# Optimization experiments

Hardware: AMD Instinct MI355X
Metric: run time of the kernel (lower is better)

The kernel has to match this reference:

```python
import jax, jax.numpy as jnp
import numpy as np

N, C, H, W = 32, 256, 56, 56
LN_EPS = 1e-5


def make_dct_filters(c, h, w):
    # Multi-spectral DCT pooling filters (FcaNet-style), bnumfre=4 frequency pairs,
    # channels split into 4 equal groups. DctCFea source unavailable; this is the
    # standard implementation pattern for such a module.
    freqs = [(0, 0), (0, 1), (1, 0), (1, 1)]
    cpf = c // len(freqs)
    f = np.zeros((c, h, w), np.float32)
    for i, (u, v) in enumerate(freqs):
        bh = np.cos(np.pi * u * (np.arange(h) + 0.5) / h) / np.sqrt(h)
        if u != 0:
            bh = bh * np.sqrt(2.0)
        bw = np.cos(np.pi * v * (np.arange(w) + 0.5) / w) / np.sqrt(w)
        if v != 0:
            bw = bw * np.sqrt(2.0)
        f[i * cpf:(i + 1) * cpf] = (bh[:, None] * bw[None, :]).astype(np.float32)
    return jnp.asarray(f)


DCT_F = make_dct_filters(C, H, W)  # (C,H,W) constant buffer


def _ln(s, g, b):
    # LayerNorm over the channel dim (normalized_shape [C,1] / [C,1,1] -> stats over C)
    mu = s.mean(axis=1, keepdims=True)
    var = ((s - mu) ** 2).mean(axis=1, keepdims=True)
    return (s - mu) * jax.lax.rsqrt(var + LN_EPS) * g + b


def setup_inputs() -> dict:
    key = jax.random.key(0)
    ks = jax.random.split(key, 8)
    return {
        "x": jax.random.normal(ks[0], (N, C, H, W), dtype=jnp.float32),
        "gc_w": jax.random.normal(ks[1], (C,), dtype=jnp.float32) * 0.02,
        "gc_b": jnp.zeros((), dtype=jnp.float32),
        "lc_w": jax.random.normal(ks[2], (3,), dtype=jnp.float32) * 0.3,
        "lc_b": jnp.zeros((), dtype=jnp.float32),
        "lcln_g": jnp.ones((C,), dtype=jnp.float32),
        "lcln_b": jnp.zeros((C,), dtype=jnp.float32),
        "tw_w": jax.random.normal(ks[3], (C, C), dtype=jnp.float32) * 0.02,
        "tw_b": jnp.zeros((C,), dtype=jnp.float32),
        "twln_g": jnp.ones((C,), dtype=jnp.float32),
        "twln_b": jnp.zeros((C,), dtype=jnp.float32),
        "wdct": jnp.full((C,), 0.5, dtype=jnp.float32),
        "wmax": jnp.full((C,), 0.5, dtype=jnp.float32),
    }


def reference(x, gc_w, gc_b, lc_w, lc_b, lcln_g, lcln_b, tw_w, tw_b, twln_g, twln_b, wdct, wmax):
    n, c, h, w = x.shape
    xf = x.reshape(n, c, h * w)                                   # (N,C,HW)
    # global context: 1x1 conv to 1 channel, softmax over space, weighted spatial sum
    logits = jnp.einsum('ncs,c->ns', xf, gc_w) + gc_b             # (N,HW)
    attn = jax.nn.softmax(logits, axis=-1)
    x_g = jnp.einsum('ncs,ns->nc', xf, attn)                      # (N,C)
    # pooled stats: max pool + DCT multi-spectral pool, learned blend
    x_max = xf.max(axis=-1)                                       # (N,C)
    x_dct = jnp.einsum('nchw,chw->nc', x, DCT_F)                  # (N,C)
    x_s = wmax * x_max + wdct * x_dct                             # (N,C)
    # local conv1d (k=3, pad=1) across the channel axis
    p = jnp.pad(x_s, ((0, 0), (1, 1)))
    x_l = lc_w[0] * p[:, :-2] + lc_w[1] * p[:, 1:-1] + lc_w[2] * p[:, 2:] + lc_b
    # LayerNorm over channels, 1x1 transform, LayerNorm, sigmoid gate
    att = _ln(x_g + x_s + x_l, lcln_g, lcln_b)                    # (N,C)
    att = att @ tw_w.T + tw_b                                     # tw: 1x1 conv C->C
    gate = jax.nn.sigmoid(_ln(att, twln_g, twln_b))               # (N,C)
    return x * gate[:, :, None, None]
```

## Files before the change

### kernel.cpp

```cpp
#include <hip/hip_runtime.h>
#include <math.h>


#define N_ 32
#define C_ 256
#define H_ 56
#define W_ 56
#define S_ 3136
#define Q_ 784
#define LN_EPS 1e-5f

#define NCH 8
#define CPC 32

using f4 = __attribute__((ext_vector_type(4))) float;

__device__ __forceinline__ float wave_sum(float v) {
  #pragma unroll
  for (int o = 32; o > 0; o >>= 1) v += __shfl_xor(v, o);
  return v;
}
__device__ __forceinline__ float wave_max(float v) {
  #pragma unroll
  for (int o = 32; o > 0; o >>= 1) v = fmaxf(v, __shfl_xor(v, o));
  return v;
}
__device__ __forceinline__ float block_sum(float v, float* red) {
  int lane = threadIdx.x & 63, wid = threadIdx.x >> 6;
  float w = wave_sum(v);
  __syncthreads();
  if (lane == 0) red[wid] = w;
  __syncthreads();
  return red[0] + red[1] + red[2] + red[3];
}
__device__ __forceinline__ float dot4(f4 a, f4 b) {
  return a.x * b.x + a.y * b.y + a.z * b.z + a.w * b.w;
}
__device__ __forceinline__ float max4(f4 a) {
  return fmaxf(fmaxf(a.x, a.y), fmaxf(a.z, a.w));
}

__global__ void k_logits(const float* __restrict__ x, const float* __restrict__ gc_w,
                         float* __restrict__ lpart) {
  int ch = blockIdx.x, n = blockIdx.y, tid = threadIdx.x;
  int c0 = ch * CPC;
  __shared__ float gw[CPC];
  if (tid < CPC) gw[tid] = gc_w[c0 + tid];
  __syncthreads();
  const f4* xb = (const f4*)(x + ((size_t)n * C_ + c0) * S_);
  f4 a0 = {0,0,0,0}, a1 = {0,0,0,0}, a2 = {0,0,0,0};
  #pragma unroll 8
  for (int c = 0; c < CPC; ++c) {
    const f4* xp = xb + (size_t)c * Q_;
    float w = gw[c];
    a0 += w * xp[tid];
    a1 += w * xp[tid + 256];
    a2 += w * xp[tid + 512];
  }
  f4* lp = (f4*)lpart + ((size_t)n * NCH + ch) * Q_;
  lp[tid] = a0; lp[tid + 256] = a1; lp[tid + 512] = a2;
  if (tid < 16) {
    f4 a3 = {0,0,0,0};
    #pragma unroll 8
    for (int c = 0; c < CPC; ++c) a3 += gw[c] * xb[(size_t)c * Q_ + 768 + tid];
    lp[768 + tid] = a3;
  }
}

__global__ void k_softmax(const float* __restrict__ lpart, float* __restrict__ attn) {
  int n = blockIdx.x, tid = threadIdx.x;
  __shared__ float red[4];
  const f4* lp = (const f4*)lpart + (size_t)n * NCH * Q_;
  f4 v[4];
  float m = -INFINITY;
  #pragma unroll
  for (int k = 0; k < 3; ++k) {
    int q = tid + k * 256;
    f4 acc = {0,0,0,0};
    #pragma unroll
    for (int ch = 0; ch < NCH; ++ch) acc += lp[(size_t)ch * Q_ + q];
    v[k] = acc;
    m = fmaxf(m, max4(acc));
  }
  if (tid < 16) {
    f4 acc = {0,0,0,0};
    #pragma unroll
    for (int ch = 0; ch < NCH; ++ch) acc += lp[(size_t)ch * Q_ + 768 + tid];
    v[3] = acc;
    m = fmaxf(m, max4(acc));
  } else {
    v[3] = f4{-INFINITY, -INFINITY, -INFINITY, -INFINITY};
  }
  float wm = wave_max(m);
  int lane = tid & 63, wid = tid >> 6;
  if (lane == 0) red[wid] = wm;
  __syncthreads();
  m = fmaxf(fmaxf(red[0], red[1]), fmaxf(red[2], red[3]));
  float z = 0.f;
  #pragma unroll
  for (int k = 0; k < 4; ++k) {
    v[k].x = expf(v[k].x - m); v[k].y = expf(v[k].y - m);
    v[k].z = expf(v[k].z - m); v[k].w = expf(v[k].w - m);
    z += v[k].x + v[k].y + v[k].z + v[k].w;
  }
  z = block_sum(z, red);
  float inv = 1.f / z;
  f4* ap = (f4*)attn + (size_t)n * Q_;
  #pragma unroll
  for (int k = 0; k < 3; ++k) ap[tid + k * 256] = v[k] * inv;
  if (tid < 16) ap[768 + tid] = v[3] * inv;
}

__global__ void k_stats(const float* __restrict__ x, const float* __restrict__ attn,
                        float* __restrict__ xg, float* __restrict__ xmax,
                        float* __restrict__ xdct) {
  int c = blockIdx.x, n = blockIdx.y, tid = threadIdx.x;
  __shared__ float bh[H_];
  __shared__ f4 bw4[14];
  __shared__ float red[3][4];
  int grp = c >> 6;
  int u = grp >> 1, vv = grp & 1;
  const float invs = 0.13363062f;
  const float sq2  = 1.41421356f;
  if (tid < H_) {
    float b = cosf((float)M_PI * u * (tid + 0.5f) / H_) * invs;
    bh[tid] = u ? b * sq2 : b;
  } else if (tid >= 64 && tid < 64 + 14) {
    int j = tid - 64;
    f4 b;
    #pragma unroll
    for (int e = 0; e < 4; ++e) {
      float t = cosf((float)M_PI * vv * (4 * j + e + 0.5f) / W_) * invs;
      ((float*)&b)[e] = vv ? t * sq2 : t;
    }
    bw4[j] = b;
  }
  __syncthreads();
  const f4* xp = (const f4*)(x + ((size_t)n * C_ + c) * S_);
  const f4* ap = (const f4*)(attn + (size_t)n * S_);
  float g = 0.f, d = 0.f, mx = -INFINITY;
  #pragma unroll
  for (int k = 0; k < 3; ++k) {
    int q = tid + k * 256;
    f4 xv = xp[q], av = ap[q];
    g += dot4(xv, av);
    mx = fmaxf(max4(xv), mx);
    int h = q / 14;
    d += bh[h] * dot4(xv, bw4[q - h * 14]);
  }
  if (tid < 16) {
    int q = 768 + tid;
    f4 xv = xp[q], av = ap[q];
    g += dot4(xv, av);
    mx = fmaxf(max4(xv), mx);
    int h = q / 14;
    d += bh[h] * dot4(xv, bw4[q - h * 14]);
  }
  float gs = wave_sum(g), ms = wave_max(mx), ds = wave_sum(d);
  int lane = tid & 63, wid = tid >> 6;
  if (lane == 0) { red[0][wid] = gs; red[1][wid] = ms; red[2][wid] = ds; }
  __syncthreads();
  if (tid == 0) {
    xg[n * C_ + c]   = red[0][0] + red[0][1] + red[0][2] + red[0][3];
    xmax[n * C_ + c] = fmaxf(fmaxf(red[1][0], red[1][1]), fmaxf(red[1][2], red[1][3]));
    xdct[n * C_ + c] = red[2][0] + red[2][1] + red[2][2] + red[2][3];
  }
}

__global__ void k_gate(const float* __restrict__ xg, const float* __restrict__ xmax,
                       const float* __restrict__ xdct,
                       const float* __restrict__ lc_w, const float* __restrict__ lc_b,
                       const float* __restrict__ lcln_g, const float* __restrict__ lcln_b,
                       const float* __restrict__ tw_w, const float* __restrict__ tw_b,
                       const float* __restrict__ twln_g, const float* __restrict__ twln_b,
                       const float* __restrict__ wdct, const float* __restrict__ wmax,
                       float* __restrict__ gate) {
  int n = blockIdx.x, c = threadIdx.x;
  __shared__ float xs[C_ + 2];
  __shared__ float att_s[C_];
  __shared__ float red[4];
  float g  = xg[n * C_ + c];
  float sv = wmax[c] * xmax[n * C_ + c] + wdct[c] * xdct[n * C_ + c];
  xs[c + 1] = sv;
  if (c == 0) { xs[0] = 0.f; xs[C_ + 1] = 0.f; }
  __syncthreads();
  float xl = lc_w[0] * xs[c] + lc_w[1] * xs[c + 1] + lc_w[2] * xs[c + 2] + lc_b[0];
  float t = g + sv + xl;
  float mu  = block_sum(t, red) * (1.f / C_);
  float dv  = t - mu;
  float var = block_sum(dv * dv, red) * (1.f / C_);
  float att = dv * rsqrtf(var + LN_EPS) * lcln_g[c] + lcln_b[c];
  att_s[c] = att;
  __syncthreads();
  float a2 = tw_b[c];
  const f4* wrow = (const f4*)(tw_w + c * C_);
  const f4* arow = (const f4*)att_s;
  #pragma unroll 8
  for (int k = 0; k < C_ / 4; ++k) a2 += dot4(wrow[k], arow[k]);
  float mu2  = block_sum(a2, red) * (1.f / C_);
  float d2   = a2 - mu2;
  float var2 = block_sum(d2 * d2, red) * (1.f / C_);
  float z = d2 * rsqrtf(var2 + LN_EPS) * twln_g[c] + twln_b[c];
  gate[n * C_ + c] = 1.f / (1.f + expf(-z));
}

__global__ void k_scale(const float* __restrict__ x, const float* __restrict__ gate,
                        float* __restrict__ out) {
  const f4* x4 = (const f4*)x;
  f4* o4 = (f4*)out;
  const int total = N_ * C_ * Q_;
  for (int i = blockIdx.x * blockDim.x + threadIdx.x; i < total;
       i += gridDim.x * blockDim.x) {
    int nc = i / Q_;
    float gv = gate[nc];
    f4 v = x4[i];
    v *= gv;
    o4[i] = v;
  }
}

extern "C" void kernel_launch(void* const* d_in, const int* in_sizes, int n_in,
                              void* d_out, int out_size, void* d_ws, size_t ws_size,
                              hipStream_t stream) {
  const float* x      = (const float*)d_in[0];
  const float* gc_w   = (const float*)d_in[1];
  const float* lc_w   = (const float*)d_in[3];
  const float* lc_b   = (const float*)d_in[4];
  const float* lcln_g = (const float*)d_in[5];
  const float* lcln_b = (const float*)d_in[6];
  const float* tw_w   = (const float*)d_in[7];
  const float* tw_b   = (const float*)d_in[8];
  const float* twln_g = (const float*)d_in[9];
  const float* twln_b = (const float*)d_in[10];
  const float* wdct   = (const float*)d_in[11];
  const float* wmax   = (const float*)d_in[12];
  float* out = (float*)d_out;

  float* ws    = (float*)d_ws;
  float* lpart = ws;
  float* attn  = lpart + (size_t)NCH * N_ * S_;
  float* xg    = attn + (size_t)N_ * S_;
  float* xmax_ = xg + N_ * C_;
  float* xdct_ = xmax_ + N_ * C_;
  float* gate  = xdct_ + N_ * C_;

  hipLaunchKernelGGL(k_logits, dim3(NCH, N_), dim3(256), 0, stream, x, gc_w, lpart);
  hipLaunchKernelGGL(k_softmax, dim3(N_), dim3(256), 0, stream, lpart, attn);
  hipLaunchKernelGGL(k_stats, dim3(C_, N_), dim3(256), 0, stream, x, attn, xg, xmax_, xdct_);
  hipLaunchKernelGGL(k_gate, dim3(N_), dim3(256), 0, stream,
                     xg, xmax_, xdct_, lc_w, lc_b, lcln_g, lcln_b,
                     tw_w, tw_b, twln_g, twln_b, wdct, wmax, gate);
  hipLaunchKernelGGL(k_scale, dim3(2048), dim3(256), 0, stream, x, gate, out);
}
```

Measured before the change: 88.90 us.

## Fuse all stages into one persistent kernel with software grid barriers

```diff
diff --git a/kernel.cpp b/kernel.cpp
--- a/kernel.cpp
+++ b/kernel.cpp
@@ -10,8 +10,10 @@
 #define Q_ 784
 #define LN_EPS 1e-5f
 
-#define NCH 8
-#define CPC 32
+#define NCH 16
+#define CPC 16
+#define GRID 512
+#define NTHR 256
 
 using f4 = __attribute__((ext_vector_type(4))) float;
 
@@ -40,182 +42,196 @@
   return fmaxf(fmaxf(a.x, a.y), fmaxf(a.z, a.w));
 }
 
-__global__ void k_logits(const float* __restrict__ x, const float* __restrict__ gc_w,
-                         float* __restrict__ lpart) {
-  int ch = blockIdx.x, n = blockIdx.y, tid = threadIdx.x;
-  int c0 = ch * CPC;
-  __shared__ float gw[CPC];
-  if (tid < CPC) gw[tid] = gc_w[c0 + tid];
-  __syncthreads();
-  const f4* xb = (const f4*)(x + ((size_t)n * C_ + c0) * S_);
-  f4 a0 = {0,0,0,0}, a1 = {0,0,0,0}, a2 = {0,0,0,0};
-  #pragma unroll 8
-  for (int c = 0; c < CPC; ++c) {
-    const f4* xp = xb + (size_t)c * Q_;
-    float w = gw[c];
-    a0 += w * xp[tid];
-    a1 += w * xp[tid + 256];
-    a2 += w * xp[tid + 512];
-  }
-  f4* lp = (f4*)lpart + ((size_t)n * NCH + ch) * Q_;
-  lp[tid] = a0; lp[tid + 256] = a1; lp[tid + 512] = a2;
-  if (tid < 16) {
-    f4 a3 = {0,0,0,0};
+__device__ __forceinline__ void grid_bar(unsigned* bar, unsigned target) {
+  __syncthreads();
+  if (threadIdx.x == 0) {
+    __threadfence();
+    __hip_atomic_fetch_add(bar, 1u, __ATOMIC_RELAXED, __HIP_MEMORY_SCOPE_AGENT);
+    while (__hip_atomic_load(bar, __ATOMIC_RELAXED, __HIP_MEMORY_SCOPE_AGENT) < target)
+      __builtin_amdgcn_s_sleep(2);
+    __threadfence();
+  }
+  __syncthreads();
+}
+
+__global__ __launch_bounds__(NTHR, 2)
+void k_fused(const float* __restrict__ x, const float* __restrict__ gc_w,
+             const float* __restrict__ lc_w, const float* __restrict__ lc_b,
+             const float* __restrict__ lcln_g, const float* __restrict__ lcln_b,
+             const float* __restrict__ tw_w, const float* __restrict__ tw_b,
+             const float* __restrict__ twln_g, const float* __restrict__ twln_b,
+             const float* __restrict__ wdct, const float* __restrict__ wmax,
+             float* __restrict__ out,
+             unsigned* __restrict__ bar, float* __restrict__ lpart,
+             float* __restrict__ attn, float* __restrict__ xg,
+             float* __restrict__ xmax, float* __restrict__ xdct,
+             float* __restrict__ gate) {
+  const int tid = threadIdx.x;
+  const int b = blockIdx.x;
+  const int lane = tid & 63, wid = tid >> 6;
+
+  {
+    __shared__ float bh[H_];
+    __shared__ f4 bw4[14];
+    __shared__ float gw[CPC];
+    __shared__ float red2[2][4];
+    int n = b >> 4, ch = b & 15, c0 = ch * CPC;
+    int grp = c0 >> 6;
+    int u = grp >> 1, vv = grp & 1;
+    const float invs = 0.13363062f;
+    const float sq2  = 1.41421356f;
+    if (tid < H_) {
+      float t = cosf((float)M_PI * u * (tid + 0.5f) / H_) * invs;
+      bh[tid] = u ? t * sq2 : t;
+    } else if (tid >= 64 && tid < 64 + 14) {
+      int j = tid - 64;
+      f4 t4;
+      #pragma unroll
+      for (int e = 0; e < 4; ++e) {
+        float t = cosf((float)M_PI * vv * (4 * j + e + 0.5f) / W_) * invs;
+        ((float*)&t4)[e] = vv ? t * sq2 : t;
+      }
+      bw4[j] = t4;
+    }
+    if (tid < CPC) gw[tid] = gc_w[c0 + tid];
+    __syncthreads();
+    const f4* xb = (const f4*)x + ((size_t)n * C_ + c0) * Q_;
+    f4 A0 = {0,0,0,0}, A1 = {0,0,0,0}, A2 = {0,0,0,0}, A3 = {0,0,0,0};
+    const int q0 = tid, q1 = tid + 256, q2 = tid + 512, q3 = tid + 768;
+    for (int c = 0; c < CPC; ++c) {
+      const f4* xp = xb + (size_t)c * Q_;
+      float wgt = gw[c];
+      f4 v0 = xp[q0], v1 = xp[q1], v2 = xp[q2];
+      A0 += wgt * v0; A1 += wgt * v1; A2 += wgt * v2;
+      float mx = fmaxf(fmaxf(max4(v0), max4(v1)), max4(v2));
+      float d  = bh[q0 / 14] * dot4(v0, bw4[q0 % 14])
+               + bh[q1 / 14] * dot4(v1, bw4[q1 % 14])
+               + bh[q2 / 14] * dot4(v2, bw4[q2 % 14]);
+      if (tid < 16) {
+        f4 v3 = xp[q3];
+        A3 += wgt * v3;
+        mx = fmaxf(mx, max4(v3));
+        d += bh[q3 / 14] * dot4(v3, bw4[q3 % 14]);
+      }
+      float ms = wave_max(mx), ds = wave_sum(d);
+      __syncthreads();
+      if (lane == 0) { red2[0][wid] = ms; red2[1][wid] = ds; }
+      __syncthreads();
+      if (tid == 0) {
+        xmax[n * C_ + c0 + c] = fmaxf(fmaxf(red2[0][0], red2[0][1]),
+                                      fmaxf(red2[0][2], red2[0][3]));
+        xdct[n * C_ + c0 + c] = red2[1][0] + red2[1][1] + red2[1][2] + red2[1][3];
+      }
+    }
+    f4* lp = (f4*)lpart + ((size_t)n * NCH + ch) * Q_;
+    lp[q0] = A0; lp[q1] = A1; lp[q2] = A2;
+    if (tid < 16) lp[q3] = A3;
+  }
+  grid_bar(bar, 1 * GRID);
+
+  if (b < N_) {
+    __shared__ float redm[4];
+    int n = b;
+    const f4* lp = (const f4*)lpart + (size_t)n * NCH * Q_;
+    f4 v[4];
+    float m = -INFINITY;
+    #pragma unroll
+    for (int k = 0; k < 3; ++k) {
+      int q = tid + k * 256;
+      f4 acc = {0,0,0,0};
+      #pragma unroll
+      for (int ch = 0; ch < NCH; ++ch) acc += lp[(size_t)ch * Q_ + q];
+      v[k] = acc;
+      m = fmaxf(m, max4(acc));
+    }
+    if (tid < 16) {
+      f4 acc = {0,0,0,0};
+      #pragma unroll
+      for (int ch = 0; ch < NCH; ++ch) acc += lp[(size_t)ch * Q_ + 768 + tid];
+      v[3] = acc;
+      m = fmaxf(m, max4(acc));
+    } else {
+      v[3] = f4{-INFINITY, -INFINITY, -INFINITY, -INFINITY};
+    }
+    float wm = wave_max(m);
+    if (lane == 0) redm[wid] = wm;
+    __syncthreads();
+    m = fmaxf(fmaxf(redm[0], redm[1]), fmaxf(redm[2], redm[3]));
+    float z = 0.f;
+    #pragma unroll
+    for (int k = 0; k < 4; ++k) {
+      v[k].x = expf(v[k].x - m); v[k].y = expf(v[k].y - m);
+      v[k].z = expf(v[k].z - m); v[k].w = expf(v[k].w - m);
+      z += v[k].x + v[k].y + v[k].z + v[k].w;
+    }
+    z = block_sum(z, redm);
+    float inv = 1.f / z;
+    f4* ap = (f4*)attn + (size_t)n * Q_;
+    #pragma unroll
+    for (int k = 0; k < 3; ++k) ap[tid + k * 256] = v[k] * inv;
+    if (tid < 16) ap[768 + tid] = v[3] * inv;
+  }
+  grid_bar(bar, 2 * GRID);
+
+  {
+    __shared__ float red1[4];
+    #pragma unroll 1
+    for (int i = 0; i < 16; ++i) {
+      int t = b * 16 + i;
+      int n = t >> 8, c = t & 255;
+      const f4* xp = (const f4*)x + ((size_t)n * C_ + c) * Q_;
+      const f4* ap = (const f4*)attn + (size_t)n * Q_;
+      float g = 0.f;
+      #pragma unroll
+      for (int k = 0; k < 3; ++k) { int q = tid + k * 256; g += dot4(xp[q], ap[q]); }
+      if (tid < 16) g += dot4(xp[768 + tid], ap[768 + tid]);
+      g = block_sum(g, red1);
+      if (tid == 0) xg[n * C_ + c] = g;
+    }
+  }
+  grid_bar(bar, 3 * GRID);
+
+  if (b < N_) {
+    __shared__ float xs[C_ + 2];
+    __shared__ float att_s[C_];
+    __shared__ float redg[4];
+    int n = b, c = tid;
+    float g  = xg[n * C_ + c];
+    float sv = wmax[c] * xmax[n * C_ + c] + wdct[c] * xdct[n * C_ + c];
+    xs[c + 1] = sv;
+    if (c == 0) { xs[0] = 0.f; xs[C_ + 1] = 0.f; }
+    __syncthreads();
+    float xl = lc_w[0] * xs[c] + lc_w[1] * xs[c + 1] + lc_w[2] * xs[c + 2] + lc_b[0];
+    float t = g + sv + xl;
+    float mu  = block_sum(t, redg) * (1.f / C_);
+    float dv  = t - mu;
+    float var = block_sum(dv * dv, redg) * (1.f / C_);
+    float att = dv * rsqrtf(var + LN_EPS) * lcln_g[c] + lcln_b[c];
+    att_s[c] = att;
+    __syncthreads();
+    float a2 = tw_b[c];
+    const f4* wrow = (const f4*)(tw_w + c * C_);
+    const f4* arow = (const f4*)att_s;
     #pragma unroll 8
-    for (int c = 0; c < CPC; ++c) a3 += gw[c] * xb[(size_t)c * Q_ + 768 + tid];
-    lp[768 + tid] = a3;
-  }
-}
-
-__global__ void k_softmax(const float* __restrict__ lpart, float* __restrict__ attn) {
-  int n = blockIdx.x, tid = threadIdx.x;
-  __shared__ float red[4];
-  const f4* lp = (const f4*)lpart + (size_t)n * NCH * Q_;
-  f4 v[4];
-  float m = -INFINITY;
-  #pragma unroll
-  for (int k = 0; k < 3; ++k) {
-    int q = tid + k * 256;
-    f4 acc = {0,0,0,0};
-    #pragma unroll
-    for (int ch = 0; ch < NCH; ++ch) acc += lp[(size_t)ch * Q_ + q];
-    v[k] = acc;
-    m = fmaxf(m, max4(acc));
-  }
-  if (tid < 16) {
-    f4 acc = {0,0,0,0};
-    #pragma unroll
-    for (int ch = 0; ch < NCH; ++ch) acc += lp[(size_t)ch * Q_ + 768 + tid];
-    v[3] = acc;
-    m = fmaxf(m, max4(acc));
-  } else {
-    v[3] = f4{-INFINITY, -INFINITY, -INFINITY, -INFINITY};
-  }
-  float wm = wave_max(m);
-  int lane = tid & 63, wid = tid >> 6;
-  if (lane == 0) red[wid] = wm;
-  __syncthreads();
-  m = fmaxf(fmaxf(red[0], red[1]), fmaxf(red[2], red[3]));
-  float z = 0.f;
-  #pragma unroll
-  for (int k = 0; k < 4; ++k) {
-    v[k].x = expf(v[k].x - m); v[k].y = expf(v[k].y - m);
-    v[k].z = expf(v[k].z - m); v[k].w = expf(v[k].w - m);
-    z += v[k].x + v[k].y + v[k].z + v[k].w;
-  }
-  z = block_sum(z, red);
-  float inv = 1.f / z;
-  f4* ap = (f4*)attn + (size_t)n * Q_;
-  #pragma unroll
-  for (int k = 0; k < 3; ++k) ap[tid + k * 256] = v[k] * inv;
-  if (tid < 16) ap[768 + tid] = v[3] * inv;
-}
-
-__global__ void k_stats(const float* __restrict__ x, const float* __restrict__ attn,
-                        float* __restrict__ xg, float* __restrict__ xmax,
-                        float* __restrict__ xdct) {
-  int c = blockIdx.x, n = blockIdx.y, tid = threadIdx.x;
-  __shared__ float bh[H_];
-  __shared__ f4 bw4[14];
-  __shared__ float red[3][4];
-  int grp = c >> 6;
-  int u = grp >> 1, vv = grp & 1;
-  const float invs = 0.13363062f;
-  const float sq2  = 1.41421356f;
-  if (tid < H_) {
-    float b = cosf((float)M_PI * u * (tid + 0.5f) / H_) * invs;
-    bh[tid] = u ? b * sq2 : b;
-  } else if (tid >= 64 && tid < 64 + 14) {
-    int j = tid - 64;
-    f4 b;
-    #pragma unroll
-    for (int e = 0; e < 4; ++e) {
-      float t = cosf((float)M_PI * vv * (4 * j + e + 0.5f) / W_) * invs;
-      ((float*)&b)[e] = vv ? t * sq2 : t;
-    }
-    bw4[j] = b;
-  }
-  __syncthreads();
-  const f4* xp = (const f4*)(x + ((size_t)n * C_ + c) * S_);
-  const f4* ap = (const f4*)(attn + (size_t)n * S_);
-  float g = 0.f, d = 0.f, mx = -INFINITY;
-  #pragma unroll
-  for (int k = 0; k < 3; ++k) {
-    int q = tid + k * 256;
-    f4 xv = xp[q], av = ap[q];
-    g += dot4(xv, av);
-    mx = fmaxf(max4(xv), mx);
-    int h = q / 14;
-    d += bh[h] * dot4(xv, bw4[q - h * 14]);
-  }
-  if (tid < 16) {
-    int q = 768 + tid;
-    f4 xv = xp[q], av = ap[q];
-    g += dot4(xv, av);
-    mx = fmaxf(max4(xv), mx);
-    int h = q / 14;
-    d += bh[h] * dot4(xv, bw4[q - h * 14]);
-  }
-  float gs = wave_sum(g), ms = wave_max(mx), ds = wave_sum(d);
-  int lane = tid & 63, wid = tid >> 6;
-  if (lane == 0) { red[0][wid] = gs; red[1][wid] = ms; red[2][wid] = ds; }
-  __syncthreads();
-  if (tid == 0) {
-    xg[n * C_ + c]   = red[0][0] + red[0][1] + red[0][2] + red[0][3];
-    xmax[n * C_ + c] = fmaxf(fmaxf(red[1][0], red[1][1]), fmaxf(red[1][2], red[1][3]));
-    xdct[n * C_ + c] = red[2][0] + red[2][1] + red[2][2] + red[2][3];
-  }
-}
-
-__global__ void k_gate(const float* __restrict__ xg, const float* __restrict__ xmax,
-                       const float* __restrict__ xdct,
-                       const float* __restrict__ lc_w, const float* __restrict__ lc_b,
-                       const float* __restrict__ lcln_g, const float* __restrict__ lcln_b,
-                       const float* __restrict__ tw_w, const float* __restrict__ tw_b,
-                       const float* __restrict__ twln_g, const float* __restrict__ twln_b,
-                       const float* __restrict__ wdct, const float* __restrict__ wmax,
-                       float* __restrict__ gate) {
-  int n = blockIdx.x, c = threadIdx.x;
-  __shared__ float xs[C_ + 2];
-  __shared__ float att_s[C_];
-  __shared__ float red[4];
-  float g  = xg[n * C_ + c];
-  float sv = wmax[c] * xmax[n * C_ + c] + wdct[c] * xdct[n * C_ + c];
-  xs[c + 1] = sv;
-  if (c == 0) { xs[0] = 0.f; xs[C_ + 1] = 0.f; }
-  __syncthreads();
-  float xl = lc_w[0] * xs[c] + lc_w[1] * xs[c + 1] + lc_w[2] * xs[c + 2] + lc_b[0];
-  float t = g + sv + xl;
-  float mu  = block_sum(t, red) * (1.f / C_);
-  float dv  = t - mu;
-  float var = block_sum(dv * dv, red) * (1.f / C_);
-  float att = dv * rsqrtf(var + LN_EPS) * lcln_g[c] + lcln_b[c];
-  att_s[c] = att;
-  __syncthreads();
-  float a2 = tw_b[c];
-  const f4* wrow = (const f4*)(tw_w + c * C_);
-  const f4* arow = (const f4*)att_s;
-  #pragma unroll 8
-  for (int k = 0; k < C_ / 4; ++k) a2 += dot4(wrow[k], arow[k]);
-  float mu2  = block_sum(a2, red) * (1.f / C_);
-  float d2   = a2 - mu2;
-  float var2 = block_sum(d2 * d2, red) * (1.f / C_);
-  float z = d2 * rsqrtf(var2 + LN_EPS) * twln_g[c] + twln_b[c];
-  gate[n * C_ + c] = 1.f / (1.f + expf(-z));
-}
-
-__global__ void k_scale(const float* __restrict__ x, const float* __restrict__ gate,
-                        float* __restrict__ out) {
-  const f4* x4 = (const f4*)x;
-  f4* o4 = (f4*)out;
-  const int total = N_ * C_ * Q_;
-  for (int i = blockIdx.x * blockDim.x + threadIdx.x; i < total;
-       i += gridDim.x * blockDim.x) {
-    int nc = i / Q_;
-    float gv = gate[nc];
-    f4 v = x4[i];
-    v *= gv;
-    o4[i] = v;
+    for (int k = 0; k < C_ / 4; ++k) a2 += dot4(wrow[k], arow[k]);
+    float mu2  = block_sum(a2, redg) * (1.f / C_);
+    float d2   = a2 - mu2;
+    float var2 = block_sum(d2 * d2, redg) * (1.f / C_);
+    float z = d2 * rsqrtf(var2 + LN_EPS) * twln_g[c] + twln_b[c];
+    gate[n * C_ + c] = 1.f / (1.f + expf(-z));
+  }
+  grid_bar(bar, 4 * GRID);
+
+  {
+    const f4* x4 = (const f4*)x;
+    f4* o4 = (f4*)out;
+    const int total = N_ * C_ * Q_;
+    for (int i = b * NTHR + tid; i < total; i += GRID * NTHR) {
+      float gv = gate[i / Q_];
+      f4 v = x4[i];
+      v *= gv;
+      o4[i] = v;
+    }
   }
 }
 
@@ -236,19 +252,18 @@
   const float* wmax   = (const float*)d_in[12];
   float* out = (float*)d_out;
 
-  float* ws    = (float*)d_ws;
-  float* lpart = ws;
-  float* attn  = lpart + (size_t)NCH * N_ * S_;
-  float* xg    = attn + (size_t)N_ * S_;
-  float* xmax_ = xg + N_ * C_;
-  float* xdct_ = xmax_ + N_ * C_;
-  float* gate  = xdct_ + N_ * C_;
-
-  hipLaunchKernelGGL(k_logits, dim3(NCH, N_), dim3(256), 0, stream, x, gc_w, lpart);
-  hipLaunchKernelGGL(k_softmax, dim3(N_), dim3(256), 0, stream, lpart, attn);
-  hipLaunchKernelGGL(k_stats, dim3(C_, N_), dim3(256), 0, stream, x, attn, xg, xmax_, xdct_);
-  hipLaunchKernelGGL(k_gate, dim3(N_), dim3(256), 0, stream,
-                     xg, xmax_, xdct_, lc_w, lc_b, lcln_g, lcln_b,
-                     tw_w, tw_b, twln_g, twln_b, wdct, wmax, gate);
-  hipLaunchKernelGGL(k_scale, dim3(2048), dim3(256), 0, stream, x, gate, out);
-}
+  float* ws = (float*)d_ws;
+  unsigned* bar = (unsigned*)ws;
+  float* lpart  = ws + 64;
+  float* attn   = lpart + (size_t)NCH * N_ * S_;
+  float* xg     = attn + (size_t)N_ * S_;
+  float* xmax_  = xg + N_ * C_;
+  float* xdct_  = xmax_ + N_ * C_;
+  float* gate   = xdct_ + N_ * C_;
+
+  (void)hipMemsetAsync(bar, 0, 256, stream);
+  hipLaunchKernelGGL(k_fused, dim3(GRID), dim3(NTHR), 0, stream,
+                     x, gc_w, lc_w, lc_b, lcln_g, lcln_b,
+                     tw_b ? tw_w : tw_w, tw_b, twln_g, twln_b, wdct, wmax,
+                     out, bar, lpart, attn, xg, xmax_, xdct_, gate);
+}
```

After: 255.4 us. 187% more time.

## Fuse max and DCT pooling into logits pass, slim stats kernel to xg only

Applied to the files above, without the earlier changes.

```diff
diff --git a/kernel.cpp b/kernel.cpp
--- a/kernel.cpp
+++ b/kernel.cpp
@@ -10,8 +10,8 @@
 #define Q_ 784
 #define LN_EPS 1e-5f
 
-#define NCH 8
-#define CPC 32
+#define NCH 16
+#define CPC 16
 
 using f4 = __attribute__((ext_vector_type(4))) float;
 
@@ -40,30 +40,80 @@
   return fmaxf(fmaxf(a.x, a.y), fmaxf(a.z, a.w));
 }
 
-__global__ void k_logits(const float* __restrict__ x, const float* __restrict__ gc_w,
-                         float* __restrict__ lpart) {
+__global__ __launch_bounds__(256)
+void k1_pool(const float* __restrict__ x, const float* __restrict__ gc_w,
+             float* __restrict__ lpart, float* __restrict__ xmax,
+             float* __restrict__ xdct) {
   int ch = blockIdx.x, n = blockIdx.y, tid = threadIdx.x;
   int c0 = ch * CPC;
   __shared__ float gw[CPC];
+  __shared__ float bh[H_];
+  __shared__ f4 bw4[14];
+  __shared__ float redm[4][CPC], redd[4][CPC];
+  int grp = c0 >> 6;
+  int u = grp >> 1, vv = grp & 1;
+  const float invs = 0.13363062f;
+  const float sq2  = 1.41421356f;
+  if (tid < H_) {
+    float t = cosf((float)M_PI * u * (tid + 0.5f) / H_) * invs;
+    bh[tid] = u ? t * sq2 : t;
+  } else if (tid >= 64 && tid < 64 + 14) {
+    int j = tid - 64;
+    f4 t4;
+    #pragma unroll
+    for (int e = 0; e < 4; ++e) {
+      float t = cosf((float)M_PI * vv * (4 * j + e + 0.5f) / W_) * invs;
+      ((float*)&t4)[e] = vv ? t * sq2 : t;
+    }
+    bw4[j] = t4;
+  }
   if (tid < CPC) gw[tid] = gc_w[c0 + tid];
   __syncthreads();
-  const f4* xb = (const f4*)(x + ((size_t)n * C_ + c0) * S_);
-  f4 a0 = {0,0,0,0}, a1 = {0,0,0,0}, a2 = {0,0,0,0};
-  #pragma unroll 8
+
+  const int q0 = tid, q1 = tid + 256, q2 = tid + 512, q3 = tid + 768;
+  const bool has3 = (tid < 16);
+  float bh0 = bh[q0 / 14], bh1 = bh[q1 / 14], bh2 = bh[q2 / 14];
+  f4 bw0 = bw4[q0 % 14], bw1 = bw4[q1 % 14], bw2 = bw4[q2 % 14];
+  float bh3 = 0.f; f4 bw3 = {0,0,0,0};
+  if (has3) { bh3 = bh[q3 / 14]; bw3 = bw4[q3 % 14]; }
+
+  const f4* xb = (const f4*)x + ((size_t)n * C_ + c0) * Q_;
+  f4 A0 = {0,0,0,0}, A1 = {0,0,0,0}, A2 = {0,0,0,0}, A3 = {0,0,0,0};
+  float mx[CPC], dc[CPC];
+  #pragma unroll
   for (int c = 0; c < CPC; ++c) {
     const f4* xp = xb + (size_t)c * Q_;
-    float w = gw[c];
-    a0 += w * xp[tid];
-    a1 += w * xp[tid + 256];
-    a2 += w * xp[tid + 512];
+    float wgt = gw[c];
+    f4 v0 = xp[q0], v1 = xp[q1], v2 = xp[q2];
+    A0 += wgt * v0; A1 += wgt * v1; A2 += wgt * v2;
+    float m = fmaxf(fmaxf(max4(v0), max4(v1)), max4(v2));
+    float d = bh0 * dot4(v0, bw0) + bh1 * dot4(v1, bw1) + bh2 * dot4(v2, bw2);
+    if (has3) {
+      f4 v3 = xp[q3];
+      A3 += wgt * v3;
+      m = fmaxf(m, max4(v3));
+      d += bh3 * dot4(v3, bw3);
+    }
+    mx[c] = m; dc[c] = d;
   }
   f4* lp = (f4*)lpart + ((size_t)n * NCH + ch) * Q_;
-  lp[tid] = a0; lp[tid + 256] = a1; lp[tid + 512] = a2;
-  if (tid < 16) {
-    f4 a3 = {0,0,0,0};
-    #pragma unroll 8
-    for (int c = 0; c < CPC; ++c) a3 += gw[c] * xb[(size_t)c * Q_ + 768 + tid];
-    lp[768 + tid] = a3;
+  lp[q0] = A0; lp[q1] = A1; lp[q2] = A2;
+  if (has3) lp[q3] = A3;
+
+  int lane = tid & 63, wid = tid >> 6;
+  #pragma unroll
+  for (int c = 0; c < CPC; ++c) {
+    float m = wave_max(mx[c]);
+    float d = wave_sum(dc[c]);
+    if (lane == 0) { redm[wid][c] = m; redd[wid][c] = d; }
+  }
+  __syncthreads();
+  if (tid < CPC) {
+    float m = fmaxf(fmaxf(redm[0][tid], redm[1][tid]),
+                    fmaxf(redm[2][tid], redm[3][tid]));
+    float d = redd[0][tid] + redd[1][tid] + redd[2][tid] + redd[3][tid];
+    xmax[n * C_ + c0 + tid] = m;
+    xdct[n * C_ + c0 + tid] = d;
   }
 }
 
@@ -111,60 +161,18 @@
   if (tid < 16) ap[768 + tid] = v[3] * inv;
 }
 
-__global__ void k_stats(const float* __restrict__ x, const float* __restrict__ attn,
-                        float* __restrict__ xg, float* __restrict__ xmax,
-                        float* __restrict__ xdct) {
+__global__ void k3_xg(const float* __restrict__ x, const float* __restrict__ attn,
+                      float* __restrict__ xg) {
   int c = blockIdx.x, n = blockIdx.y, tid = threadIdx.x;
-  __shared__ float bh[H_];
-  __shared__ f4 bw4[14];
-  __shared__ float red[3][4];
-  int grp = c >> 6;
-  int u = grp >> 1, vv = grp & 1;
-  const float invs = 0.13363062f;
-  const float sq2  = 1.41421356f;
-  if (tid < H_) {
-    float b = cosf((float)M_PI * u * (tid + 0.5f) / H_) * invs;
-    bh[tid] = u ? b * sq2 : b;
-  } else if (tid >= 64 && tid < 64 + 14) {
-    int j = tid - 64;
-    f4 b;
-    #pragma unroll
-    for (int e = 0; e < 4; ++e) {
-      float t = cosf((float)M_PI * vv * (4 * j + e + 0.5f) / W_) * invs;
-      ((float*)&b)[e] = vv ? t * sq2 : t;
-    }
-    bw4[j] = b;
-  }
-  __syncthreads();
-  const f4* xp = (const f4*)(x + ((size_t)n * C_ + c) * S_);
-  const f4* ap = (const f4*)(attn + (size_t)n * S_);
-  float g = 0.f, d = 0.f, mx = -INFINITY;
-  #pragma unroll
-  for (int k = 0; k < 3; ++k) {
-    int q = tid + k * 256;
-    f4 xv = xp[q], av = ap[q];
-    g += dot4(xv, av);
-    mx = fmaxf(max4(xv), mx);
-    int h = q / 14;
-    d += bh[h] * dot4(xv, bw4[q - h * 14]);
-  }
-  if (tid < 16) {
-    int q = 768 + tid;
-    f4 xv = xp[q], av = ap[q];
-    g += dot4(xv, av);
-    mx = fmaxf(max4(xv), mx);
-    int h = q / 14;
-    d += bh[h] * dot4(xv, bw4[q - h * 14]);
-  }
-  float gs = wave_sum(g), ms = wave_max(mx), ds = wave_sum(d);
-  int lane = tid & 63, wid = tid >> 6;
-  if (lane == 0) { red[0][wid] = gs; red[1][wid] = ms; red[2][wid] = ds; }
-  __syncthreads();
-  if (tid == 0) {
-    xg[n * C_ + c]   = red[0][0] + red[0][1] + red[0][2] + red[0][3];
-    xmax[n * C_ + c] = fmaxf(fmaxf(red[1][0], red[1][1]), fmaxf(red[1][2], red[1][3]));
-    xdct[n * C_ + c] = red[2][0] + red[2][1] + red[2][2] + red[2][3];
-  }
+  __shared__ float red[4];
+  const f4* xp = (const f4*)x + ((size_t)n * C_ + c) * Q_;
+  const f4* ap = (const f4*)attn + (size_t)n * Q_;
+  float g = 0.f;
+  #pragma unroll
+  for (int k = 0; k < 3; ++k) { int q = tid + k * 256; g += dot4(xp[q], ap[q]); }
+  if (tid < 16) g += dot4(xp[768 + tid], ap[768 + tid]);
+  g = block_sum(g, red);
+  if (tid == 0) xg[n * C_ + c] = g;
 }
 
 __global__ void k_gate(const float* __restrict__ xg, const float* __restrict__ xmax,
@@ -244,9 +252,10 @@
   float* xdct_ = xmax_ + N_ * C_;
   float* gate  = xdct_ + N_ * C_;
 
-  hipLaunchKernelGGL(k_logits, dim3(NCH, N_), dim3(256), 0, stream, x, gc_w, lpart);
+  hipLaunchKernelGGL(k1_pool, dim3(NCH, N_), dim3(256), 0, stream,
+                     x, gc_w, lpart, xmax_, xdct_);
   hipLaunchKernelGGL(k_softmax, dim3(N_), dim3(256), 0, stream, lpart, attn);
-  hipLaunchKernelGGL(k_stats, dim3(C_, N_), dim3(256), 0, stream, x, attn, xg, xmax_, xdct_);
+  hipLaunchKernelGGL(k3_xg, dim3(C_, N_), dim3(256), 0, stream, x, attn, xg);
   hipLaunchKernelGGL(k_gate, dim3(N_), dim3(256), 0, stream,
                      xg, xmax_, xdct_, lc_w, lc_b, lcln_g, lcln_b,
                      tw_w, tw_b, twln_g, twln_b, wdct, wmax, gate);
```

After: 109.2 us. 1.23x slower.
